# Optimization experiments

Measured on AMD Instinct MI355X. Metric: run time of the kernel, lower is better.

Reference implementation:

```python
import jax, jax.numpy as jnp
import numpy as np

N_HEAD = 8
LINEAR_DIM = 64
IN_PIXELS = 4096  # h*w = 64*64
D = N_HEAD * LINEAR_DIM  # 512
C = 128
LN_EPS = 1e-6
BN_EPS = 1e-5


def setup_inputs() -> dict:
    key = jax.random.key(0)
    ks = jax.random.split(key, 10)
    shp = (16, C, 64, 64)
    # Kaiming-uniform-ish small init for weights (torch Linear weight layout: [out, in])
    def lin(k, out_f, in_f):
        lim = 1.0 / np.sqrt(in_f)
        return jax.random.uniform(k, (out_f, in_f), jnp.float32, -lim, lim)
    return {
        "v": jax.random.normal(ks[0], shp, jnp.float32),
        "k": jax.random.normal(ks[1], shp, jnp.float32),
        "q": jax.random.normal(ks[2], shp, jnp.float32),
        "w_qs": lin(ks[3], D, IN_PIXELS),
        "w_ks": lin(ks[4], D, IN_PIXELS),
        "w_vs": lin(ks[5], D, IN_PIXELS),
        "w_fc": lin(ks[6], IN_PIXELS, D),
        "ln_gamma": jnp.ones((D,), jnp.float32),
        "ln_beta": jnp.zeros((D,), jnp.float32),
        "temperature": jnp.asarray(IN_PIXELS ** 0.5, jnp.float32),
        "bn_gamma": jnp.ones((C,), jnp.float32),
        "bn_beta": jnp.zeros((C,), jnp.float32),
    }


def _layer_norm(x, gamma, beta):
    # torch-faithful: unbiased std (ddof=1), divide by (std + eps)
    mean = jnp.mean(x, axis=-1, keepdims=True)
    var = jnp.var(x, axis=-1, keepdims=True, ddof=1)
    std = jnp.sqrt(var)
    return gamma * (x - mean) / (std + LN_EPS) + beta


def reference(v, k, q, w_qs, w_ks, w_vs, w_fc, ln_gamma, ln_beta, temperature, bn_gamma, bn_beta):
    b, c, h, w = q.shape
    P = h * w
    qf = q.reshape(b, c, P)
    kf = k.reshape(b, c, P)
    vf = v.reshape(b, c, P)
    residual = vf
    # QKV projections: [b,c,P] @ W^T -> [b,c,D] -> [b,nh,c,ld]
    def proj(x, W):
        y = jnp.einsum('bcp,dp->bcd', x, W)
        return y.reshape(b, c, N_HEAD, LINEAR_DIM).transpose(0, 2, 1, 3)
    Q = proj(qf, w_qs)
    K = proj(kf, w_ks)
    V = proj(vf, w_vs)
    # channel-wise attention: scores [b,nh,c,c]
    scores = jnp.einsum('bhcd,bhed->bhce', Q / temperature, K)
    attn = jax.nn.softmax(scores, axis=-1)
    O = jnp.einsum('bhce,bhed->bhcd', attn, V)
    O = O.transpose(0, 2, 1, 3).reshape(b, c, N_HEAD * LINEAR_DIM)
    # Swish -> LayerNorm -> fc -> residual
    O = O * jax.nn.sigmoid(O)
    O = _layer_norm(O, ln_gamma, ln_beta)
    O = jnp.einsum('bcd,pd->bcp', O, w_fc)
    out = (residual + O).reshape(b, c, h, w)
    # BatchNorm2d in training mode: batch stats over (b,h,w), biased variance
    mean = jnp.mean(out, axis=(0, 2, 3), keepdims=True)
    var = jnp.var(out, axis=(0, 2, 3), keepdims=True)
    out = (out - mean) / jnp.sqrt(var + BN_EPS)
    out = out * bn_gamma[None, :, None, None] + bn_beta[None, :, None, None]
    return out
```

## Files before the change

### kernel.cpp

```cpp
#include <hip/hip_runtime.h>
#include <hip/hip_bf16.h>
#include <stdint.h>

typedef __attribute__((ext_vector_type(8))) short bf16x8;
typedef __attribute__((ext_vector_type(4))) float f32x4;

#define AS1(p) ((const __attribute__((address_space(1))) uint32_t*)(p))
#define AS3(p) ((__attribute__((address_space(3))) uint32_t*)(p))

__device__ __forceinline__ ushort f2bf(float f) {
  uint32_t u = __float_as_uint(f);
  uint32_t r = (u + 0x7fffu + ((u >> 16) & 1u)) >> 16;
  return (ushort)r;
}

__device__ __forceinline__ float bf2f(ushort u) {
  uint32_t v = ((uint32_t)u) << 16;
  return __uint_as_float(v);
}

__device__ __forceinline__ uint4 cvt8u(float4 a0, float4 a1) {
  uint4 r;
  asm("v_cvt_pk_bf16_f32 %0, %1, %2" : "=v"(r.x) : "v"(a0.x), "v"(a0.y));
  asm("v_cvt_pk_bf16_f32 %0, %1, %2" : "=v"(r.y) : "v"(a0.z), "v"(a0.w));
  asm("v_cvt_pk_bf16_f32 %0, %1, %2" : "=v"(r.z) : "v"(a1.x), "v"(a1.y));
  asm("v_cvt_pk_bf16_f32 %0, %1, %2" : "=v"(r.w) : "v"(a1.z), "v"(a1.w));
  return r;
}

__global__ __launch_bounds__(256) void pack4(
    const float* __restrict__ s0, const float* __restrict__ s1,
    const float* __restrict__ s2, const float* __restrict__ s3,
    ushort* __restrict__ o0, ushort* __restrict__ o1,
    ushort* __restrict__ o2, ushort* __restrict__ o3, int n)
{
  const float* s; ushort* o;
  switch (blockIdx.y) {
    case 0: s = s0; o = o0; break;
    case 1: s = s1; o = o1; break;
    case 2: s = s2; o = o2; break;
    default: s = s3; o = o3; break;
  }
  int stride = gridDim.x * 1024;
  for (int i = (blockIdx.x * 256 + threadIdx.x) * 4; i < n; i += stride) {
    float4 v = *(const float4*)(s + i);
    ushort4 u;
    u.x = f2bf(v.x); u.y = f2bf(v.y); u.z = f2bf(v.z); u.w = f2bf(v.w);
    *(ushort4*)(o + i) = u;
  }
}

__global__ __launch_bounds__(256, 3) void gemm_qkv(
    const float* __restrict__ aq, const float* __restrict__ ak, const float* __restrict__ av,
    const ushort* __restrict__ wq, const ushort* __restrict__ wk, const ushort* __restrict__ wv,
    ushort* __restrict__ part, int lgs)
{
  __shared__ __align__(16) ushort At[128 * 64];
  __shared__ __align__(16) ushort Bt[128 * 64];
  int per = gridDim.x >> 3;
  int bid = blockIdx.x;
  int swz = (bid & 7) * per + (bid >> 3);
  int y = swz & 3, x = (swz >> 2) & 15, zz = swz >> 6;
  int g = zz >> lgs, s = zz & ((1 << lgs) - 1);
  const float* A; const ushort* Bm;
  if (g == 0)      { A = aq; Bm = wq; }
  else if (g == 1) { A = ak; Bm = wk; }
  else             { A = av; Bm = wv; }
  ushort* Pd = part + ((size_t)zz) * 1048576;
  const int K = 4096;
  const int kchunk = K >> lgs;
  const int k0 = s * kchunk, kend = k0 + kchunk;
  int rowBase = x * 128;
  int colBase = y * 128;
  int tid = threadIdx.x, l = tid & 63, w = tid >> 6;
  int wr = w >> 1, wc = w & 1, fr = l & 15, fq = l >> 4;

  int arow = tid >> 3;
  int aslot = tid & 7;
  int aswz = aslot ^ (arow & 7);
  const float* Abase = A + (size_t)(rowBase + arow) * K + aslot * 8;
  char* At0 = (char*)At + arow * 128 + aswz * 16;

  f32x4 acc[4][4];
#pragma unroll
  for (int m = 0; m < 4; ++m)
#pragma unroll
    for (int n = 0; n < 4; ++n) acc[m][n] = (f32x4){0.f, 0.f, 0.f, 0.f};

  float4 a0, a1, a2, a3, a4, a5, a6, a7;

#define LOADA(ktn) do { \
    a0 = *(const float4*)(Abase + (size_t)0 * K + (ktn)); \
    a1 = *(const float4*)(Abase + (size_t)0 * K + (ktn) + 4); \
    a2 = *(const float4*)(Abase + (size_t)32 * K + (ktn)); \
    a3 = *(const float4*)(Abase + (size_t)32 * K + (ktn) + 4); \
    a4 = *(const float4*)(Abase + (size_t)64 * K + (ktn)); \
    a5 = *(const float4*)(Abase + (size_t)64 * K + (ktn) + 4); \
    a6 = *(const float4*)(Abase + (size_t)96 * K + (ktn)); \
    a7 = *(const float4*)(Abase + (size_t)96 * K + (ktn) + 4); \
  } while (0)

#define CVTWRITEA do { \
    *(uint4*)(At0 + 0 * 4096)  = cvt8u(a0, a1); \
    *(uint4*)(At0 + 1 * 4096)  = cvt8u(a2, a3); \
    *(uint4*)(At0 + 2 * 4096)  = cvt8u(a4, a5); \
    *(uint4*)(At0 + 3 * 4096)  = cvt8u(a6, a7); \
  } while (0)

#define STAGEB(ktn) do { \
    _Pragma("unroll") \
    for (int j = 0; j < 4; ++j) { \
      int c = ((w * 4 + j) << 6) + l; \
      int row = c >> 3, slot = c & 7; \
      int srccol = (slot ^ (row & 7)) * 8; \
      __builtin_amdgcn_global_load_lds(AS1(Bm + (size_t)(colBase + row) * K + (ktn) + srccol), \
                                       AS3((char*)Bt + c * 16), 16, 0, 0); \
    } \
  } while (0)

#define MFMAPHASE do { \
    _Pragma("unroll") \
    for (int kc = 0; kc < 2; ++kc) { \
      bf16x8 af[4], bv[4]; \
      _Pragma("unroll") \
      for (int m = 0; m < 4; ++m) { \
        int r = wr * 64 + m * 16 + fr; \
        int sl = (kc * 4 + fq) ^ (fr & 7); \
        af[m] = *(const bf16x8*)((const char*)At + r * 128 + sl * 16); \
      } \
      _Pragma("unroll") \
      for (int n = 0; n < 4; ++n) { \
        int r = wc * 64 + n * 16 + fr; \
        int sl = (kc * 4 + fq) ^ (fr & 7); \
        bv[n] = *(const bf16x8*)((const char*)Bt + r * 128 + sl * 16); \
      } \
      _Pragma("unroll") \
      for (int m = 0; m < 4; ++m) \
        _Pragma("unroll") \
        for (int n = 0; n < 4; ++n) \
          acc[m][n] = __builtin_amdgcn_mfma_f32_16x16x32_bf16(af[m], bv[n], acc[m][n], 0, 0, 0); \
    } \
  } while (0)

  LOADA(k0);
  STAGEB(k0);

#pragma unroll 1
  for (int kt = k0; kt < kend; kt += 64) {
    CVTWRITEA;
    __syncthreads();
    MFMAPHASE;
    __syncthreads();
    if (kt + 64 < kend) {
      LOADA(kt + 64);
      STAGEB(kt + 64);
    }
  }

#undef LOADA
#undef CVTWRITEA
#undef STAGEB
#undef MFMAPHASE

#pragma unroll
  for (int m = 0; m < 4; ++m)
#pragma unroll
    for (int n = 0; n < 4; ++n)
#pragma unroll
      for (int r = 0; r < 4; ++r) {
        int row = rowBase + wr * 64 + m * 16 + fq * 4 + r;
        int col = colBase + wc * 64 + n * 16 + fr;
        Pd[(size_t)row * 512 + col] = f2bf(acc[m][n][r]);
      }
}

__global__ __launch_bounds__(256) void reduce_qkv(
    const ushort* __restrict__ part, ushort* __restrict__ Qp, ushort* __restrict__ Kp,
    ushort* __restrict__ Vp, int lgs)
{
  int g = blockIdx.y;
  ushort* dst = g == 0 ? Qp : (g == 1 ? Kp : Vp);
  const ushort* p = part + (((size_t)g) << lgs) * 1048576;
  int i = (blockIdx.x * 256 + threadIdx.x) * 8;
  int splits = 1 << lgs;
  float accv[8];
  {
    bf16x8 v = *(const bf16x8*)(p + i);
#pragma unroll
    for (int j = 0; j < 8; ++j) accv[j] = bf2f((ushort)v[j]);
  }
  for (int s = 1; s < splits; ++s) {
    bf16x8 v = *(const bf16x8*)(p + (size_t)s * 1048576 + i);
#pragma unroll
    for (int j = 0; j < 8; ++j) accv[j] += bf2f((ushort)v[j]);
  }
  ushort u[8];
#pragma unroll
  for (int j = 0; j < 8; ++j) u[j] = f2bf(accv[j]);
  *(uint4*)(dst + i) = *(uint4*)u;
}

__global__ __launch_bounds__(256) void attn(
    const ushort* __restrict__ Qp, const ushort* __restrict__ Kp, const ushort* __restrict__ Vp,
    float* __restrict__ Obuf, const float* __restrict__ temp)
{
  __shared__ __align__(16) ushort Qs[64 * 64];
  __shared__ __align__(16) ushort Ks[128 * 64];
  __shared__ __align__(16) ushort Vt[64 * 128];
  __shared__ __align__(16) float  Sl[64 * 128];
  __shared__ __align__(16) ushort Pl[64 * 128];
  __shared__ float rsum[64];
  int bh = blockIdx.y, b = bh >> 3, h = bh & 7;
  int c0 = blockIdx.x * 64;
  int tid = threadIdx.x, l = tid & 63, w = tid >> 6;
  int wr = w >> 1, wc = w & 1, fr = l & 15, fq = l >> 4;
  float invT = 1.0f / temp[0];
  const size_t rowQ = (size_t)(b * 128 + c0);

#pragma unroll
  for (int j = 0; j < 2; ++j) {
    int c = ((w * 2 + j) << 6) + l, row = c >> 3, cc = c & 7;
    __builtin_amdgcn_global_load_lds(AS1(Qp + (rowQ + row) * 512 + h * 64 + cc * 8),
                                     AS3((char*)Qs + (w * 2 + j) * 1024), 16, 0, 0);
  }
#pragma unroll
  for (int j = 0; j < 4; ++j) {
    int c = ((w * 4 + j) << 6) + l, row = c >> 3, cc = c & 7;
    __builtin_amdgcn_global_load_lds(AS1(Kp + (size_t)(b * 128 + row) * 512 + h * 64 + cc * 8),
                                     AS3((char*)Ks + (w * 4 + j) * 1024), 16, 0, 0);
  }
#pragma unroll
  for (int t = 0; t < 4; ++t) {
    int ch = tid + t * 256, e = ch >> 3, d0 = (ch & 7) * 8;
    bf16x8 vv = *(const bf16x8*)(Vp + (size_t)(b * 128 + e) * 512 + h * 64 + d0);
#pragma unroll
    for (int j = 0; j < 8; ++j) Vt[(d0 + j) * 128 + e] = (ushort)vv[j];
  }
  __syncthreads();

  f32x4 sa[2][4];
#pragma unroll
  for (int m = 0; m < 2; ++m)
#pragma unroll
    for (int n = 0; n < 4; ++n) sa[m][n] = (f32x4){0.f, 0.f, 0.f, 0.f};
#pragma unroll
  for (int kc = 0; kc < 2; ++kc) {
    bf16x8 aQ[2], bK[4];
#pragma unroll
    for (int m = 0; m < 2; ++m)
      aQ[m] = *(const bf16x8*)&Qs[(wr * 32 + m * 16 + fr) * 64 + kc * 32 + fq * 8];
#pragma unroll
    for (int n = 0; n < 4; ++n)
      bK[n] = *(const bf16x8*)&Ks[(wc * 64 + n * 16 + fr) * 64 + kc * 32 + fq * 8];
#pragma unroll
    for (int m = 0; m < 2; ++m)
#pragma unroll
      for (int n = 0; n < 4; ++n)
        sa[m][n] = __builtin_amdgcn_mfma_f32_16x16x32_bf16(aQ[m], bK[n], sa[m][n], 0, 0, 0);
  }
#pragma unroll
  for (int m = 0; m < 2; ++m)
#pragma unroll
    for (int n = 0; n < 4; ++n)
#pragma unroll
      for (int r = 0; r < 4; ++r)
        Sl[(wr * 32 + m * 16 + fq * 4 + r) * 128 + wc * 64 + n * 16 + fr] = sa[m][n][r] * invT;
  __syncthreads();

  {
    int row = tid >> 2, qq = tid & 3;
    const float* srow = Sl + row * 128 + qq * 32;
    float4 va[8];
#pragma unroll
    for (int i = 0; i < 8; ++i) va[i] = *(const float4*)(srow + i * 4);
    float mx = -1e30f;
#pragma unroll
    for (int i = 0; i < 8; ++i)
      mx = fmaxf(mx, fmaxf(fmaxf(va[i].x, va[i].y), fmaxf(va[i].z, va[i].w)));
    mx = fmaxf(mx, __shfl_xor(mx, 1));
    mx = fmaxf(mx, __shfl_xor(mx, 2));
    float ssum = 0.f;
    ushort* prow = Pl + row * 128 + qq * 32;
#pragma unroll
    for (int i = 0; i < 8; ++i) {
      float e0 = __expf(va[i].x - mx), e1 = __expf(va[i].y - mx);
      float e2 = __expf(va[i].z - mx), e3 = __expf(va[i].w - mx);
      ssum += (e0 + e1) + (e2 + e3);
      ushort4 u; u.x = f2bf(e0); u.y = f2bf(e1); u.z = f2bf(e2); u.w = f2bf(e3);
      *(ushort4*)(prow + i * 4) = u;
    }
    ssum += __shfl_xor(ssum, 1);
    ssum += __shfl_xor(ssum, 2);
    if (qq == 0) rsum[row] = ssum;
  }
  __syncthreads();

  f32x4 oa[2][2];
#pragma unroll
  for (int m = 0; m < 2; ++m)
#pragma unroll
    for (int n = 0; n < 2; ++n) oa[m][n] = (f32x4){0.f, 0.f, 0.f, 0.f};
#pragma unroll
  for (int kc = 0; kc < 4; ++kc) {
    bf16x8 aP[2], bV[2];
#pragma unroll
    for (int m = 0; m < 2; ++m)
      aP[m] = *(const bf16x8*)&Pl[(wr * 32 + m * 16 + fr) * 128 + kc * 32 + fq * 8];
#pragma unroll
    for (int n = 0; n < 2; ++n)
      bV[n] = *(const bf16x8*)&Vt[(wc * 32 + n * 16 + fr) * 128 + kc * 32 + fq * 8];
#pragma unroll
    for (int m = 0; m < 2; ++m)
#pragma unroll
      for (int n = 0; n < 2; ++n)
        oa[m][n] = __builtin_amdgcn_mfma_f32_16x16x32_bf16(aP[m], bV[n], oa[m][n], 0, 0, 0);
  }
#pragma unroll
  for (int m = 0; m < 2; ++m)
#pragma unroll
    for (int n = 0; n < 2; ++n)
#pragma unroll
      for (int r = 0; r < 4; ++r) {
        int row = wr * 32 + m * 16 + fq * 4 + r, col = wc * 32 + n * 16 + fr;
        Obuf[(rowQ + row) * 512 + h * 64 + col] = oa[m][n][r] / rsum[row];
      }
}

__global__ __launch_bounds__(256) void swish_ln(
    const float* __restrict__ O, ushort* __restrict__ X,
    const float* __restrict__ gamma, const float* __restrict__ beta)
{
  int row = blockIdx.x * 4 + (threadIdx.x >> 6);
  int lane = threadIdx.x & 63;
  const float* x = O + (size_t)row * 512 + lane * 8;
  float4 va = *(const float4*)(x);
  float4 vb = *(const float4*)(x + 4);
  float y[8] = {va.x, va.y, va.z, va.w, vb.x, vb.y, vb.z, vb.w};
  float s = 0.f, sq = 0.f;
#pragma unroll
  for (int i = 0; i < 8; ++i) {
    y[i] = y[i] / (1.f + __expf(-y[i]));
    s += y[i]; sq += y[i] * y[i];
  }
#pragma unroll
  for (int o = 1; o < 64; o <<= 1) { s += __shfl_xor(s, o); sq += __shfl_xor(sq, o); }
  float mean = s * (1.f / 512.f);
  float var = (sq - s * mean) * (1.f / 511.f);
  float inv = 1.f / (sqrtf(var) + 1e-6f);
  const float4 g0 = *(const float4*)(gamma + lane * 8);
  const float4 g1 = *(const float4*)(gamma + lane * 8 + 4);
  const float4 b0 = *(const float4*)(beta + lane * 8);
  const float4 b1 = *(const float4*)(beta + lane * 8 + 4);
  float gg[8] = {g0.x, g0.y, g0.z, g0.w, g1.x, g1.y, g1.z, g1.w};
  float bb[8] = {b0.x, b0.y, b0.z, b0.w, b1.x, b1.y, b1.z, b1.w};
  ushort u[8];
#pragma unroll
  for (int i = 0; i < 8; ++i) u[i] = f2bf(gg[i] * (y[i] - mean) * inv + bb[i]);
  *(uint4*)(X + (size_t)row * 512 + lane * 8) = *(uint4*)u;
}

__global__ __launch_bounds__(256) void gemm_fc(
    const ushort* __restrict__ A, const ushort* __restrict__ Bm,
    const float* __restrict__ resid, ushort* __restrict__ valb,
    float* __restrict__ bn_sum, float* __restrict__ bn_sq)
{
  __shared__ __align__(16) ushort At[128 * 64];
  __shared__ __align__(16) ushort Bt[128 * 64];
  __shared__ float csum[128], csq[128];
  const int K = 512;
  int rowBase = blockIdx.x * 128;
  int colBase = blockIdx.y * 128;
  int tid = threadIdx.x, l = tid & 63, w = tid >> 6;
  int wr = w >> 1, wc = w & 1, fr = l & 15, fq = l >> 4;
  if (tid < 128) { csum[tid] = 0.f; csq[tid] = 0.f; }
  f32x4 acc[4][4];
#pragma unroll
  for (int m = 0; m < 4; ++m)
#pragma unroll
    for (int n = 0; n < 4; ++n) acc[m][n] = (f32x4){0.f, 0.f, 0.f, 0.f};

  for (int kt = 0; kt < K; kt += 64) {
#pragma unroll
    for (int j = 0; j < 4; ++j) {
      int c = ((w * 4 + j) << 6) + l;
      int row = c >> 3, cc = c & 7;
      __builtin_amdgcn_global_load_lds(AS1(A + (size_t)(rowBase + row) * K + kt + cc * 8),
                                       AS3((char*)At + (w * 4 + j) * 1024), 16, 0, 0);
      __builtin_amdgcn_global_load_lds(AS1(Bm + (size_t)(colBase + row) * K + kt + cc * 8),
                                       AS3((char*)Bt + (w * 4 + j) * 1024), 16, 0, 0);
    }
    __syncthreads();
#pragma unroll
    for (int kc = 0; kc < 2; ++kc) {
      bf16x8 af[4], bfv[4];
#pragma unroll
      for (int m = 0; m < 4; ++m)
        af[m] = *(const bf16x8*)&At[(wr * 64 + m * 16 + fr) * 64 + kc * 32 + fq * 8];
#pragma unroll
      for (int n = 0; n < 4; ++n)
        bfv[n] = *(const bf16x8*)&Bt[(wc * 64 + n * 16 + fr) * 64 + kc * 32 + fq * 8];
#pragma unroll
      for (int m = 0; m < 4; ++m)
#pragma unroll
        for (int n = 0; n < 4; ++n)
          acc[m][n] = __builtin_amdgcn_mfma_f32_16x16x32_bf16(af[m], bfv[n], acc[m][n], 0, 0, 0);
    }
    __syncthreads();
  }
#pragma unroll
  for (int m = 0; m < 4; ++m)
#pragma unroll
    for (int r = 0; r < 4; ++r) {
      float ps = 0.f, pq = 0.f;
#pragma unroll
      for (int n = 0; n < 4; ++n) {
        int row = rowBase + wr * 64 + m * 16 + fq * 4 + r;
        int col = colBase + wc * 64 + n * 16 + fr;
        size_t idx = (size_t)row * 4096 + col;
        float val = acc[m][n][r] + resid[idx];
        valb[idx] = f2bf(val);
        ps += val; pq += val * val;
      }
#pragma unroll
      for (int o = 1; o < 16; o <<= 1) { ps += __shfl_xor(ps, o); pq += __shfl_xor(pq, o); }
      if (fr == 0) {
        int ch = wr * 64 + m * 16 + fq * 4 + r;
        atomicAdd(&csum[ch], ps);
        atomicAdd(&csq[ch], pq);
      }
    }
  __syncthreads();
  if (tid < 128) {
    atomicAdd(&bn_sum[tid], csum[tid]);
    atomicAdd(&bn_sq[tid], csq[tid]);
  }
}

__global__ __launch_bounds__(256) void bn_norm(
    const ushort* __restrict__ valb, float* __restrict__ out,
    const float* __restrict__ bn_sum, const float* __restrict__ bn_sq,
    const float* __restrict__ gamma, const float* __restrict__ beta)
{
  __shared__ float sc[128], sh[128];
  const float inv_n = 1.f / 65536.f;
  int tid = threadIdx.x;
  if (tid < 128) {
    float mean = bn_sum[tid] * inv_n;
    float var = bn_sq[tid] * inv_n - mean * mean;
    float g = gamma[tid] * rsqrtf(var + 1e-5f);
    sc[tid] = g;
    sh[tid] = beta[tid] - mean * g;
  }
  __syncthreads();
  int stride = gridDim.x * blockDim.x;
  for (int v = blockIdx.x * blockDim.x + tid; v < 1048576; v += stride) {
    int elem = v * 8;
    int ch = (elem >> 12) & 127;
    float g = sc[ch], bta = sh[ch];
    bf16x8 x = *(const bf16x8*)(valb + elem);
    float4 o0, o1;
    o0.x = bf2f((ushort)x[0]) * g + bta;
    o0.y = bf2f((ushort)x[1]) * g + bta;
    o0.z = bf2f((ushort)x[2]) * g + bta;
    o0.w = bf2f((ushort)x[3]) * g + bta;
    o1.x = bf2f((ushort)x[4]) * g + bta;
    o1.y = bf2f((ushort)x[5]) * g + bta;
    o1.z = bf2f((ushort)x[6]) * g + bta;
    o1.w = bf2f((ushort)x[7]) * g + bta;
    *(float4*)(out + elem) = o0;
    *(float4*)(out + elem + 4) = o1;
  }
}

extern "C" void kernel_launch(void* const* d_in, const int* in_sizes, int n_in,
                              void* d_out, int out_size, void* d_ws, size_t ws_size,
                              hipStream_t stream)
{
  const float* v_in = (const float*)d_in[0];
  const float* k_in = (const float*)d_in[1];
  const float* q_in = (const float*)d_in[2];
  const float* w_qs = (const float*)d_in[3];
  const float* w_ks = (const float*)d_in[4];
  const float* w_vs = (const float*)d_in[5];
  const float* w_fc = (const float*)d_in[6];
  const float* ln_g = (const float*)d_in[7];
  const float* ln_b = (const float*)d_in[8];
  const float* temp = (const float*)d_in[9];
  const float* bn_g = (const float*)d_in[10];
  const float* bn_b = (const float*)d_in[11];
  float* out = (float*)d_out;

  char* ws = (char*)d_ws;
  size_t off = 0;
  auto alloc = [&](size_t bytes) { char* p = ws + off; off += bytes; return p; };
  ushort* wq  = (ushort*)alloc(512ull * 4096 * 2);
  ushort* wk  = (ushort*)alloc(512ull * 4096 * 2);
  ushort* wv  = (ushort*)alloc(512ull * 4096 * 2);
  ushort* wfc = (ushort*)alloc(512ull * 4096 * 2);
  ushort* Qp  = (ushort*)alloc(2048ull * 512 * 2);
  ushort* Kp  = (ushort*)alloc(2048ull * 512 * 2);
  ushort* Vp  = (ushort*)alloc(2048ull * 512 * 2);
  float*  Obuf= (float*)alloc(2048ull * 512 * 4);
  ushort* X16 = (ushort*)alloc(2048ull * 512 * 2);
  ushort* valb= (ushort*)alloc(2048ull * 4096 * 2);
  float*  bns = (float*)alloc(128 * 4);
  float*  bnq = (float*)alloc(128 * 4);

  int lgs = 3;
  while (lgs > 0 && off + (3ull << lgs) * 1048576 * 2 > ws_size) --lgs;
  ushort* part = (ushort*)alloc((3ull << lgs) * 1048576 * 2);

  hipMemsetAsync(bns, 0, 256 * 4, stream);

  pack4<<<dim3(512, 4), 256, 0, stream>>>(w_qs, w_ks, w_vs, w_fc, wq, wk, wv, wfc,
                                          512 * 4096);
  gemm_qkv<<<16 * 4 * (3 << lgs), 256, 0, stream>>>(q_in, k_in, v_in, wq, wk, wv, part, lgs);
  reduce_qkv<<<dim3(512, 3), 256, 0, stream>>>(part, Qp, Kp, Vp, lgs);
  attn<<<dim3(2, 128), 256, 0, stream>>>(Qp, Kp, Vp, Obuf, temp);
  swish_ln<<<512, 256, 0, stream>>>(Obuf, X16, ln_g, ln_b);
  gemm_fc<<<dim3(16, 32), 256, 0, stream>>>(X16, wfc, v_in, valb, bns, bnq);
  bn_norm<<<2048, 256, 0, stream>>>(valb, out, bns, bnq, bn_g, bn_b);
}
```

Baseline: 119.4 us.

## Fuse split-K QKV reduction into attention kernel and drop split count

Removes the separate reduce_qkv kernel: the attention kernel now sums the split-K partial products for Q, K and V while loading them into shared memory. This saves one launch and a round trip through global memory for the reduced Q/K/V. Q and K tiles are stored with an XOR swizzle to avoid LDS bank conflicts. The split count drops from 8 to 4, which halves partial traffic but gives the QKV GEMM less parallelism. K and V partials are also re-read redundantly by both attention blocks per head.

```diff
diff --git a/kernel.cpp b/kernel.cpp
--- a/kernel.cpp
+++ b/kernel.cpp
@@ -174,35 +174,9 @@
       }
 }
 
-__global__ __launch_bounds__(256) void reduce_qkv(
-    const ushort* __restrict__ part, ushort* __restrict__ Qp, ushort* __restrict__ Kp,
-    ushort* __restrict__ Vp, int lgs)
-{
-  int g = blockIdx.y;
-  ushort* dst = g == 0 ? Qp : (g == 1 ? Kp : Vp);
-  const ushort* p = part + (((size_t)g) << lgs) * 1048576;
-  int i = (blockIdx.x * 256 + threadIdx.x) * 8;
-  int splits = 1 << lgs;
-  float accv[8];
-  {
-    bf16x8 v = *(const bf16x8*)(p + i);
-#pragma unroll
-    for (int j = 0; j < 8; ++j) accv[j] = bf2f((ushort)v[j]);
-  }
-  for (int s = 1; s < splits; ++s) {
-    bf16x8 v = *(const bf16x8*)(p + (size_t)s * 1048576 + i);
-#pragma unroll
-    for (int j = 0; j < 8; ++j) accv[j] += bf2f((ushort)v[j]);
-  }
-  ushort u[8];
-#pragma unroll
-  for (int j = 0; j < 8; ++j) u[j] = f2bf(accv[j]);
-  *(uint4*)(dst + i) = *(uint4*)u;
-}
-
 __global__ __launch_bounds__(256) void attn(
-    const ushort* __restrict__ Qp, const ushort* __restrict__ Kp, const ushort* __restrict__ Vp,
-    float* __restrict__ Obuf, const float* __restrict__ temp)
+    const ushort* __restrict__ part, float* __restrict__ Obuf,
+    const float* __restrict__ temp, int lgs)
 {
   __shared__ __align__(16) ushort Qs[64 * 64];
   __shared__ __align__(16) ushort Ks[128 * 64];
@@ -216,25 +190,58 @@
   int wr = w >> 1, wc = w & 1, fr = l & 15, fq = l >> 4;
   float invT = 1.0f / temp[0];
   const size_t rowQ = (size_t)(b * 128 + c0);
-
-#pragma unroll
-  for (int j = 0; j < 2; ++j) {
-    int c = ((w * 2 + j) << 6) + l, row = c >> 3, cc = c & 7;
-    __builtin_amdgcn_global_load_lds(AS1(Qp + (rowQ + row) * 512 + h * 64 + cc * 8),
-                                     AS3((char*)Qs + (w * 2 + j) * 1024), 16, 0, 0);
-  }
-#pragma unroll
-  for (int j = 0; j < 4; ++j) {
-    int c = ((w * 4 + j) << 6) + l, row = c >> 3, cc = c & 7;
-    __builtin_amdgcn_global_load_lds(AS1(Kp + (size_t)(b * 128 + row) * 512 + h * 64 + cc * 8),
-                                     AS3((char*)Ks + (w * 4 + j) * 1024), 16, 0, 0);
+  const int splits = 1 << lgs;
+  const ushort* Pq = part;
+  const ushort* Pk = part + (((size_t)1) << lgs) * 1048576;
+  const ushort* Pv = part + (((size_t)2) << lgs) * 1048576;
+
+#pragma unroll
+  for (int t = 0; t < 2; ++t) {
+    int c = tid + t * 256;
+    int row = c >> 3, slot = c & 7;
+    size_t gidx = (rowQ + row) * 512 + h * 64 + slot * 8;
+    float qa[8] = {0.f, 0.f, 0.f, 0.f, 0.f, 0.f, 0.f, 0.f};
+#pragma unroll 1
+    for (int s = 0; s < splits; ++s) {
+      bf16x8 v = *(const bf16x8*)(Pq + (size_t)s * 1048576 + gidx);
+#pragma unroll
+      for (int j = 0; j < 8; ++j) qa[j] += bf2f((ushort)v[j]);
+    }
+    ushort u[8];
+#pragma unroll
+    for (int j = 0; j < 8; ++j) u[j] = f2bf(qa[j]);
+    *(uint4*)((char*)Qs + row * 128 + ((slot ^ (row & 7)) * 16)) = *(uint4*)u;
+  }
+#pragma unroll
+  for (int t = 0; t < 4; ++t) {
+    int c = tid + t * 256;
+    int row = c >> 3, slot = c & 7;
+    size_t gidx = (size_t)(b * 128 + row) * 512 + h * 64 + slot * 8;
+    float ka[8] = {0.f, 0.f, 0.f, 0.f, 0.f, 0.f, 0.f, 0.f};
+#pragma unroll 1
+    for (int s = 0; s < splits; ++s) {
+      bf16x8 v = *(const bf16x8*)(Pk + (size_t)s * 1048576 + gidx);
+#pragma unroll
+      for (int j = 0; j < 8; ++j) ka[j] += bf2f((ushort)v[j]);
+    }
+    ushort u[8];
+#pragma unroll
+    for (int j = 0; j < 8; ++j) u[j] = f2bf(ka[j]);
+    *(uint4*)((char*)Ks + row * 128 + ((slot ^ (row & 7)) * 16)) = *(uint4*)u;
   }
 #pragma unroll
   for (int t = 0; t < 4; ++t) {
     int ch = tid + t * 256, e = ch >> 3, d0 = (ch & 7) * 8;
-    bf16x8 vv = *(const bf16x8*)(Vp + (size_t)(b * 128 + e) * 512 + h * 64 + d0);
-#pragma unroll
-    for (int j = 0; j < 8; ++j) Vt[(d0 + j) * 128 + e] = (ushort)vv[j];
+    size_t gidx = (size_t)(b * 128 + e) * 512 + h * 64 + d0;
+    float va[8] = {0.f, 0.f, 0.f, 0.f, 0.f, 0.f, 0.f, 0.f};
+#pragma unroll 1
+    for (int s = 0; s < splits; ++s) {
+      bf16x8 v = *(const bf16x8*)(Pv + (size_t)s * 1048576 + gidx);
+#pragma unroll
+      for (int j = 0; j < 8; ++j) va[j] += bf2f((ushort)v[j]);
+    }
+#pragma unroll
+    for (int j = 0; j < 8; ++j) Vt[(d0 + j) * 128 + e] = f2bf(va[j]);
   }
   __syncthreads();
 
@@ -247,11 +254,17 @@
   for (int kc = 0; kc < 2; ++kc) {
     bf16x8 aQ[2], bK[4];
 #pragma unroll
-    for (int m = 0; m < 2; ++m)
-      aQ[m] = *(const bf16x8*)&Qs[(wr * 32 + m * 16 + fr) * 64 + kc * 32 + fq * 8];
-#pragma unroll
-    for (int n = 0; n < 4; ++n)
-      bK[n] = *(const bf16x8*)&Ks[(wc * 64 + n * 16 + fr) * 64 + kc * 32 + fq * 8];
+    for (int m = 0; m < 2; ++m) {
+      int r = wr * 32 + m * 16 + fr;
+      int sl = (kc * 4 + fq) ^ (r & 7);
+      aQ[m] = *(const bf16x8*)((const char*)Qs + r * 128 + sl * 16);
+    }
+#pragma unroll
+    for (int n = 0; n < 4; ++n) {
+      int r = wc * 64 + n * 16 + fr;
+      int sl = (kc * 4 + fq) ^ (r & 7);
+      bK[n] = *(const bf16x8*)((const char*)Ks + r * 128 + sl * 16);
+    }
 #pragma unroll
     for (int m = 0; m < 2; ++m)
 #pragma unroll
@@ -497,16 +510,13 @@
   ushort* wk  = (ushort*)alloc(512ull * 4096 * 2);
   ushort* wv  = (ushort*)alloc(512ull * 4096 * 2);
   ushort* wfc = (ushort*)alloc(512ull * 4096 * 2);
-  ushort* Qp  = (ushort*)alloc(2048ull * 512 * 2);
-  ushort* Kp  = (ushort*)alloc(2048ull * 512 * 2);
-  ushort* Vp  = (ushort*)alloc(2048ull * 512 * 2);
   float*  Obuf= (float*)alloc(2048ull * 512 * 4);
   ushort* X16 = (ushort*)alloc(2048ull * 512 * 2);
   ushort* valb= (ushort*)alloc(2048ull * 4096 * 2);
   float*  bns = (float*)alloc(128 * 4);
   float*  bnq = (float*)alloc(128 * 4);
 
-  int lgs = 3;
+  int lgs = 2;
   while (lgs > 0 && off + (3ull << lgs) * 1048576 * 2 > ws_size) --lgs;
   ushort* part = (ushort*)alloc((3ull << lgs) * 1048576 * 2);
 
@@ -515,8 +525,7 @@
   pack4<<<dim3(512, 4), 256, 0, stream>>>(w_qs, w_ks, w_vs, w_fc, wq, wk, wv, wfc,
                                           512 * 4096);
   gemm_qkv<<<16 * 4 * (3 << lgs), 256, 0, stream>>>(q_in, k_in, v_in, wq, wk, wv, part, lgs);
-  reduce_qkv<<<dim3(512, 3), 256, 0, stream>>>(part, Qp, Kp, Vp, lgs);
-  attn<<<dim3(2, 128), 256, 0, stream>>>(Qp, Kp, Vp, Obuf, temp);
+  attn<<<dim3(2, 128), 256, 0, stream>>>(part, Obuf, temp, lgs);
   swish_ln<<<512, 256, 0, stream>>>(Obuf, X16, ln_g, ln_b);
   gemm_fc<<<dim3(16, 32), 256, 0, stream>>>(X16, wfc, v_in, valb, bns, bnq);
   bn_norm<<<2048, 256, 0, stream>>>(valb, out, bns, bnq, bn_g, bn_b);
```

Result: no change. 121.1 us (+1.4%).
